# Optimization experiments

Measured on AMD Instinct MI355X. Metric: run time of the kernel, lower is better.

The kernel has to match this reference:

```python
import jax, jax.numpy as jnp
import numpy as np

MAX_HOPS = 3


def setup_inputs() -> dict:
    key = jax.random.key(0)
    ks = jax.random.split(key, 6)
    B, M, S = 128, 200, 20
    V, D = 100000, 128
    NC, CL = 10000, 10
    stories = jax.random.randint(ks[0], (B, M, S), 0, V, dtype=jnp.int64)
    queries = jax.random.randint(ks[1], (B, S), 0, V, dtype=jnp.int64)
    candidates = jax.random.randint(ks[2], (NC, CL), 0, V, dtype=jnp.int64)
    # 0.05 scale keeps hop softmax logits in a sane range
    A_tab = jax.random.normal(ks[3], (V, D), dtype=jnp.float32) * 0.05
    W_tab = jax.random.normal(ks[4], (V, D), dtype=jnp.float32) * 0.05
    H_w = jax.random.normal(ks[5], (D, D), dtype=jnp.float32) * 0.05
    return {"stories": stories, "queries": queries, "candidates": candidates,
            "A_tab": A_tab, "W_tab": W_tab, "H_w": H_w}


def reference(stories, queries, candidates, A_tab, W_tab, H_w):
    # padding_idx=0: embedding row 0 is zero
    A = A_tab.at[0].set(0.0)
    W = W_tab.at[0].set(0.0)
    # query encoding: gather + sum-pool -> [B, D]
    u = jnp.sum(A[queries], axis=1)
    # memory encoding: [B, M, D] (same A table each hop, as in the source)
    m = jnp.sum(A[stories], axis=2)
    for _ in range(MAX_HOPS):
        dotted = jnp.einsum('bmd,bd->bm', m, u)          # attention logits
        probs = jax.nn.softmax(dotted, axis=1)           # [B, M]
        o = jnp.einsum('bm,bmd->bd', probs, m)           # weighted memory sum
        u = jnp.tanh(u @ H_w.T + o)                      # Linear(no bias) + tanh
    cand_sum = jnp.sum(W[candidates], axis=1)            # [NC, D]
    logits = u @ cand_sum.T                              # [B, NC]
    return logits
```

## Files before the change

### kernel.cpp

```cpp
#include <hip/hip_runtime.h>
#include <math.h>

#define BB 128
#define MM 200
#define SS 20
#define DD 128
#define NCC 10000
#define CL 10
#define LCT 64

__device__ __forceinline__ unsigned pack_bf16(float a, float b) {
    unsigned ua = __float_as_uint(a), ub = __float_as_uint(b);
    ua += 0x7fff + ((ua >> 16) & 1);
    ub += 0x7fff + ((ub >> 16) & 1);
    return (ua >> 16) | (ub & 0xffff0000u);
}
__device__ __forceinline__ float bflo(unsigned v) { return __uint_as_float(v << 16); }
__device__ __forceinline__ float bfhi(unsigned v) { return __uint_as_float(v & 0xffff0000u); }

__device__ __forceinline__ int detect_shift(const int* __restrict__ q) {
    int zc = 0;
#pragma unroll
    for (int i = 0; i < 8; ++i) zc += (q[2 * i + 1] == 0);
    return (zc >= 6) ? 1 : 0;
}

__global__ __launch_bounds__(512) void k_gather(const int* __restrict__ stories,
                                                const int* __restrict__ queries,
                                                const int* __restrict__ cands,
                                                const float* __restrict__ A,
                                                const float* __restrict__ W,
                                                unsigned* __restrict__ m_ws,
                                                float* __restrict__ cand_ws,
                                                float* __restrict__ u_ws) {
    int gid = blockIdx.x, tid = threadIdx.x;
    int shift = detect_shift(queries);
    int g = tid >> 5, l = tid & 31;

    int base = gid * 50;
#pragma unroll
    for (int r = 0; r < 4; ++r) {
        int rl = (r << 4) + g;
        if (rl < 50) {
            int row = base + rl;
            int toks[SS];
#pragma unroll
            for (int s = 0; s < SS; ++s)
                toks[s] = stories[((size_t)(row * SS + s)) << shift];
            float4 acc = make_float4(0.f, 0.f, 0.f, 0.f);
#pragma unroll
            for (int s = 0; s < SS; ++s) {
                float4 v = ((const float4*)(A + (size_t)toks[s] * DD))[l];
                float msk = toks[s] ? 1.f : 0.f;
                acc.x = fmaf(msk, v.x, acc.x);
                acc.y = fmaf(msk, v.y, acc.y);
                acc.z = fmaf(msk, v.z, acc.z);
                acc.w = fmaf(msk, v.w, acc.w);
            }
            uint2 o;
            o.x = pack_bf16(acc.x, acc.y);
            o.y = pack_bf16(acc.z, acc.w);
            ((uint2*)(m_ws + (size_t)row * (DD / 2)))[l] = o;
        }
    }
#pragma unroll
    for (int r = 0; r < 2; ++r) {
        int rl = (r << 4) + g;
        int row = gid * 20 + rl;
        if (rl < 20 && row < NCC) {
            int toks[CL];
#pragma unroll
            for (int s = 0; s < CL; ++s)
                toks[s] = cands[((size_t)(row * CL + s)) << shift];
            float4 acc = make_float4(0.f, 0.f, 0.f, 0.f);
#pragma unroll
            for (int s = 0; s < CL; ++s) {
                float4 v = ((const float4*)(W + (size_t)toks[s] * DD))[l];
                float msk = toks[s] ? 1.f : 0.f;
                acc.x = fmaf(msk, v.x, acc.x);
                acc.y = fmaf(msk, v.y, acc.y);
                acc.z = fmaf(msk, v.z, acc.z);
                acc.w = fmaf(msk, v.w, acc.w);
            }
            ((float4*)(cand_ws + (size_t)row * DD))[l] = acc;
        }
    }
    if (gid < BB && tid < 32) {
        int toks[SS];
#pragma unroll
        for (int s = 0; s < SS; ++s)
            toks[s] = queries[((size_t)(gid * SS + s)) << shift];
        float4 acc = make_float4(0.f, 0.f, 0.f, 0.f);
#pragma unroll
        for (int s = 0; s < SS; ++s) {
            float4 v = ((const float4*)(A + (size_t)toks[s] * DD))[tid];
            float msk = toks[s] ? 1.f : 0.f;
            acc.x = fmaf(msk, v.x, acc.x);
            acc.y = fmaf(msk, v.y, acc.y);
            acc.z = fmaf(msk, v.z, acc.z);
            acc.w = fmaf(msk, v.w, acc.w);
        }
        ((float4*)(u_ws + (size_t)gid * DD))[tid] = acc;
    }
}

__global__ __launch_bounds__(512) void k_hops(const unsigned* __restrict__ m_ws,
                                              const float* __restrict__ u_ws,
                                              const float* __restrict__ Hw,
                                              float* __restrict__ uT) {
    __shared__ float u_s[DD];
    __shared__ float p_s[MM];
    __shared__ float o_part[8][DD];
    __shared__ float red_s;
    int b = blockIdx.x, tid = threadIdx.x;
    int wave = tid >> 6, lane = tid & 63;
    const unsigned* mb = m_ws + (size_t)b * MM * (DD / 2);

    if (tid < DD) u_s[tid] = u_ws[b * DD + tid];
    __syncthreads();

    for (int hop = 0; hop < 3; ++hop) {
        {
            float2 uu = ((const float2*)u_s)[lane];
            for (int i = 0; i < 25; ++i) {
                int mm = wave * 25 + i;
                unsigned pv = mb[mm * (DD / 2) + lane];
                float d = bflo(pv) * uu.x + bfhi(pv) * uu.y;
                for (int off = 32; off; off >>= 1) d += __shfl_down(d, off);
                if (lane == 0) p_s[mm] = d;
            }
        }
        __syncthreads();
        if (tid < 64) {
            float v0 = p_s[tid], v1 = p_s[tid + 64], v2 = p_s[tid + 128];
            float v3 = (tid < 8) ? p_s[tid + 192] : -1e30f;
            float mx = fmaxf(fmaxf(v0, v1), fmaxf(v2, v3));
            for (int off = 32; off; off >>= 1) mx = fmaxf(mx, __shfl_down(mx, off));
            mx = __shfl(mx, 0);
            float e0 = __expf(v0 - mx), e1 = __expf(v1 - mx), e2 = __expf(v2 - mx);
            float e3 = (tid < 8) ? __expf(v3 - mx) : 0.f;
            float sm = e0 + e1 + e2 + e3;
            for (int off = 32; off; off >>= 1) sm += __shfl_down(sm, off);
            p_s[tid] = e0;
            p_s[tid + 64] = e1;
            p_s[tid + 128] = e2;
            if (tid < 8) p_s[tid + 192] = e3;
            if (tid == 0) red_s = 1.f / __shfl(sm, 0);
        }
        __syncthreads();
        {
            int c = tid & 63, h = tid >> 6;
            int mm0 = h * 25;
            float ax = 0.f, ay = 0.f;
#pragma unroll 5
            for (int k = 0; k < 25; ++k) {
                unsigned pv = mb[(mm0 + k) * (DD / 2) + c];
                float p = p_s[mm0 + k];
                ax = fmaf(p, bflo(pv), ax);
                ay = fmaf(p, bfhi(pv), ay);
            }
            o_part[h][2 * c] = ax;
            o_part[h][2 * c + 1] = ay;
        }
        __syncthreads();
        float u_new = 0.f;
        if (tid < DD) {
            float o = 0.f;
#pragma unroll
            for (int h = 0; h < 8; ++h) o += o_part[h][tid];
            float acc = o * red_s;
            const float4* hrow = (const float4*)(Hw + tid * DD);
            const float4* u4 = (const float4*)u_s;
#pragma unroll 8
            for (int j = 0; j < DD / 4; ++j) {
                float4 hv = hrow[j];
                float4 uv = u4[j];
                acc += hv.x * uv.x + hv.y * uv.y + hv.z * uv.z + hv.w * uv.w;
            }
            u_new = tanhf(acc);
        }
        __syncthreads();
        if (tid < DD) u_s[tid] = u_new;
        __syncthreads();
    }
    if (tid < DD) uT[tid * BB + b] = u_s[tid];
}

__global__ __launch_bounds__(256) void k_logits(const float* __restrict__ uT,
                                                const float* __restrict__ cs,
                                                float* __restrict__ out) {
    __shared__ float c_s[DD][LCT + 4];
    int c0 = blockIdx.x * LCT;
    int tid = threadIdx.x;
    {
        int c = tid >> 2, l = tid & 3;
        int row = c0 + c;
        if (row >= NCC) row = NCC - 1;
        const float4* rp = (const float4*)(cs + (size_t)row * DD);
#pragma unroll
        for (int i = 0; i < 8; ++i) {
            int k = (l << 5) + (i << 2);
            float4 v = rp[(l << 3) + i];
            c_s[k][c] = v.x;
            c_s[k + 1][c] = v.y;
            c_s[k + 2][c] = v.z;
            c_s[k + 3][c] = v.w;
        }
    }
    __syncthreads();
    int tx = tid & 31, ty = tid >> 5;
    const float* cb = &c_s[0][ty << 3];
    const float4* up = (const float4*)(uT + (tx << 2));
    float acc[4][8];
#pragma unroll
    for (int i = 0; i < 4; ++i)
#pragma unroll
        for (int j = 0; j < 8; ++j) acc[i][j] = 0.f;
#pragma unroll 4
    for (int k = 0; k < DD; ++k) {
        float4 uv = up[k * (BB / 4)];
        float4 ca = *(const float4*)(cb + k * (LCT + 4));
        float4 cc = *(const float4*)(cb + k * (LCT + 4) + 4);
        float uu[4] = {uv.x, uv.y, uv.z, uv.w};
        float cv[8] = {ca.x, ca.y, ca.z, ca.w, cc.x, cc.y, cc.z, cc.w};
#pragma unroll
        for (int i = 0; i < 4; ++i)
#pragma unroll
            for (int j = 0; j < 8; ++j) acc[i][j] = fmaf(uu[i], cv[j], acc[i][j]);
    }
    if (c0 + (ty << 3) < NCC) {
#pragma unroll
        for (int i = 0; i < 4; ++i) {
            float* orow = out + (size_t)((tx << 2) + i) * NCC + c0 + (ty << 3);
            ((float4*)orow)[0] = make_float4(acc[i][0], acc[i][1], acc[i][2], acc[i][3]);
            ((float4*)orow)[1] = make_float4(acc[i][4], acc[i][5], acc[i][6], acc[i][7]);
        }
    }
}

extern "C" void kernel_launch(void* const* d_in, const int* in_sizes, int n_in,
                              void* d_out, int out_size, void* d_ws, size_t ws_size,
                              hipStream_t stream) {
    const int* stories = (const int*)d_in[0];
    const int* queries = (const int*)d_in[1];
    const int* cands   = (const int*)d_in[2];
    const float* A  = (const float*)d_in[3];
    const float* W  = (const float*)d_in[4];
    const float* Hw = (const float*)d_in[5];
    float* out = (float*)d_out;

    unsigned* m_ws = (unsigned*)d_ws;
    float* cand_ws = (float*)(m_ws + (size_t)BB * MM * (DD / 2));
    float* u_ws = cand_ws + (size_t)NCC * DD;
    float* uT = u_ws + BB * DD;

    k_gather<<<512, 512, 0, stream>>>(stories, queries, cands, A, W,
                                      m_ws, cand_ws, u_ws);
    k_hops<<<BB, 512, 0, stream>>>(m_ws, u_ws, Hw, uT);
    k_logits<<<(NCC + LCT - 1) / LCT, 256, 0, stream>>>(uT, cand_ws, out);
}
```

Measured before the change: 205.6 us.

## Split gather into role-specialized blocks and batch loads in hop kernel

The gather kernel moves from 512 blocks that each loop over story, candidate and query rows to 2233 blocks, each handling 16 rows of one kind, which exposes more parallelism and removes per-block serial loops. In the hop kernel, the attention dot products are batched five rows at a time so loads and shuffle reductions interleave. The weighted-sum loop also preloads all 25 memory words into registers before accumulating. Together these aim to raise memory-level parallelism, at the cost of more registers per thread and possibly lower occupancy.

```diff
diff --git a/kernel.cpp b/kernel.cpp
--- a/kernel.cpp
+++ b/kernel.cpp
@@ -8,6 +8,11 @@
 #define NCC 10000
 #define CL 10
 #define LCT 64
+
+#define SBLK 1600
+#define CBLK 625
+#define QBLK 8
+#define GBLK (SBLK + CBLK + QBLK)
 
 __device__ __forceinline__ unsigned pack_bf16(float a, float b) {
     unsigned ua = __float_as_uint(a), ub = __float_as_uint(b);
@@ -37,70 +42,60 @@
     int shift = detect_shift(queries);
     int g = tid >> 5, l = tid & 31;
 
-    int base = gid * 50;
-#pragma unroll
-    for (int r = 0; r < 4; ++r) {
-        int rl = (r << 4) + g;
-        if (rl < 50) {
-            int row = base + rl;
-            int toks[SS];
-#pragma unroll
-            for (int s = 0; s < SS; ++s)
-                toks[s] = stories[((size_t)(row * SS + s)) << shift];
-            float4 acc = make_float4(0.f, 0.f, 0.f, 0.f);
-#pragma unroll
-            for (int s = 0; s < SS; ++s) {
-                float4 v = ((const float4*)(A + (size_t)toks[s] * DD))[l];
-                float msk = toks[s] ? 1.f : 0.f;
-                acc.x = fmaf(msk, v.x, acc.x);
-                acc.y = fmaf(msk, v.y, acc.y);
-                acc.z = fmaf(msk, v.z, acc.z);
-                acc.w = fmaf(msk, v.w, acc.w);
-            }
-            uint2 o;
-            o.x = pack_bf16(acc.x, acc.y);
-            o.y = pack_bf16(acc.z, acc.w);
-            ((uint2*)(m_ws + (size_t)row * (DD / 2)))[l] = o;
-        }
-    }
-#pragma unroll
-    for (int r = 0; r < 2; ++r) {
-        int rl = (r << 4) + g;
-        int row = gid * 20 + rl;
-        if (rl < 20 && row < NCC) {
-            int toks[CL];
-#pragma unroll
-            for (int s = 0; s < CL; ++s)
-                toks[s] = cands[((size_t)(row * CL + s)) << shift];
-            float4 acc = make_float4(0.f, 0.f, 0.f, 0.f);
-#pragma unroll
-            for (int s = 0; s < CL; ++s) {
-                float4 v = ((const float4*)(W + (size_t)toks[s] * DD))[l];
-                float msk = toks[s] ? 1.f : 0.f;
-                acc.x = fmaf(msk, v.x, acc.x);
-                acc.y = fmaf(msk, v.y, acc.y);
-                acc.z = fmaf(msk, v.z, acc.z);
-                acc.w = fmaf(msk, v.w, acc.w);
-            }
-            ((float4*)(cand_ws + (size_t)row * DD))[l] = acc;
-        }
-    }
-    if (gid < BB && tid < 32) {
+    if (gid < SBLK) {
+        int row = (gid << 4) + g;
         int toks[SS];
 #pragma unroll
         for (int s = 0; s < SS; ++s)
-            toks[s] = queries[((size_t)(gid * SS + s)) << shift];
+            toks[s] = stories[((size_t)(row * SS + s)) << shift];
         float4 acc = make_float4(0.f, 0.f, 0.f, 0.f);
 #pragma unroll
         for (int s = 0; s < SS; ++s) {
-            float4 v = ((const float4*)(A + (size_t)toks[s] * DD))[tid];
+            float4 v = ((const float4*)(A + (size_t)toks[s] * DD))[l];
             float msk = toks[s] ? 1.f : 0.f;
             acc.x = fmaf(msk, v.x, acc.x);
             acc.y = fmaf(msk, v.y, acc.y);
             acc.z = fmaf(msk, v.z, acc.z);
             acc.w = fmaf(msk, v.w, acc.w);
         }
-        ((float4*)(u_ws + (size_t)gid * DD))[tid] = acc;
+        uint2 o;
+        o.x = pack_bf16(acc.x, acc.y);
+        o.y = pack_bf16(acc.z, acc.w);
+        ((uint2*)(m_ws + (size_t)row * (DD / 2)))[l] = o;
+    } else if (gid < SBLK + CBLK) {
+        int row = ((gid - SBLK) << 4) + g;
+        int toks[CL];
+#pragma unroll
+        for (int s = 0; s < CL; ++s)
+            toks[s] = cands[((size_t)(row * CL + s)) << shift];
+        float4 acc = make_float4(0.f, 0.f, 0.f, 0.f);
+#pragma unroll
+        for (int s = 0; s < CL; ++s) {
+            float4 v = ((const float4*)(W + (size_t)toks[s] * DD))[l];
+            float msk = toks[s] ? 1.f : 0.f;
+            acc.x = fmaf(msk, v.x, acc.x);
+            acc.y = fmaf(msk, v.y, acc.y);
+            acc.z = fmaf(msk, v.z, acc.z);
+            acc.w = fmaf(msk, v.w, acc.w);
+        }
+        ((float4*)(cand_ws + (size_t)row * DD))[l] = acc;
+    } else {
+        int b = ((gid - SBLK - CBLK) << 4) + g;
+        int toks[SS];
+#pragma unroll
+        for (int s = 0; s < SS; ++s)
+            toks[s] = queries[((size_t)(b * SS + s)) << shift];
+        float4 acc = make_float4(0.f, 0.f, 0.f, 0.f);
+#pragma unroll
+        for (int s = 0; s < SS; ++s) {
+            float4 v = ((const float4*)(A + (size_t)toks[s] * DD))[l];
+            float msk = toks[s] ? 1.f : 0.f;
+            acc.x = fmaf(msk, v.x, acc.x);
+            acc.y = fmaf(msk, v.y, acc.y);
+            acc.z = fmaf(msk, v.z, acc.z);
+            acc.w = fmaf(msk, v.w, acc.w);
+        }
+        ((float4*)(u_ws + (size_t)b * DD))[l] = acc;
     }
 }
 
@@ -122,12 +117,25 @@
     for (int hop = 0; hop < 3; ++hop) {
         {
             float2 uu = ((const float2*)u_s)[lane];
-            for (int i = 0; i < 25; ++i) {
-                int mm = wave * 25 + i;
-                unsigned pv = mb[mm * (DD / 2) + lane];
-                float d = bflo(pv) * uu.x + bfhi(pv) * uu.y;
-                for (int off = 32; off; off >>= 1) d += __shfl_down(d, off);
-                if (lane == 0) p_s[mm] = d;
+#pragma unroll
+            for (int i = 0; i < 5; ++i) {
+                int mm0 = wave * 25 + i * 5;
+                unsigned pv[5];
+#pragma unroll
+                for (int k = 0; k < 5; ++k)
+                    pv[k] = mb[(mm0 + k) * (DD / 2) + lane];
+                float d[5];
+#pragma unroll
+                for (int k = 0; k < 5; ++k)
+                    d[k] = bflo(pv[k]) * uu.x + bfhi(pv[k]) * uu.y;
+#pragma unroll
+                for (int off = 32; off; off >>= 1)
+#pragma unroll
+                    for (int k = 0; k < 5; ++k) d[k] += __shfl_down(d[k], off);
+                if (lane == 0) {
+#pragma unroll
+                    for (int k = 0; k < 5; ++k) p_s[mm0 + k] = d[k];
+                }
             }
         }
         __syncthreads();
@@ -151,13 +159,16 @@
         {
             int c = tid & 63, h = tid >> 6;
             int mm0 = h * 25;
+            unsigned pv[25];
+#pragma unroll
+            for (int k = 0; k < 25; ++k)
+                pv[k] = mb[(mm0 + k) * (DD / 2) + c];
             float ax = 0.f, ay = 0.f;
-#pragma unroll 5
+#pragma unroll
             for (int k = 0; k < 25; ++k) {
-                unsigned pv = mb[(mm0 + k) * (DD / 2) + c];
                 float p = p_s[mm0 + k];
-                ax = fmaf(p, bflo(pv), ax);
-                ay = fmaf(p, bfhi(pv), ay);
+                ax = fmaf(p, bflo(pv[k]), ax);
+                ay = fmaf(p, bfhi(pv[k]), ay);
             }
             o_part[h][2 * c] = ax;
             o_part[h][2 * c + 1] = ay;
@@ -254,8 +265,8 @@
     float* u_ws = cand_ws + (size_t)NCC * DD;
     float* uT = u_ws + BB * DD;
 
-    k_gather<<<512, 512, 0, stream>>>(stories, queries, cands, A, W,
-                                      m_ws, cand_ws, u_ws);
+    k_gather<<<GBLK, 512, 0, stream>>>(stories, queries, cands, A, W,
+                                       m_ws, cand_ws, u_ws);
     k_hops<<<BB, 512, 0, stream>>>(m_ws, u_ws, Hw, uT);
     k_logits<<<(NCC + LCT - 1) / LCT, 256, 0, stream>>>(uT, cand_ws, out);
 }
```

Result: faster. 191.0 us (-7.1%).
